# Kernel tuning notes

Measured on AMD Instinct MI355X. Metric: run time of the kernel, lower is better.

Reference implementation:

```python
import jax, jax.numpy as jnp
import numpy as np

D_MODEL = 1024
NUM_HEADS = 16
HEAD_DIM = D_MODEL // NUM_HEADS


def setup_inputs() -> dict:
    key = jax.random.key(0)
    ks = jax.random.split(key, 9)
    s = 1.0 / np.sqrt(D_MODEL)
    x = jax.random.normal(ks[0], (2, 2048, D_MODEL), dtype=jnp.float32)
    Wq = jax.random.uniform(ks[1], (D_MODEL, D_MODEL), jnp.float32, -s, s)
    bq = jax.random.uniform(ks[2], (D_MODEL,), jnp.float32, -s, s)
    Wk = jax.random.uniform(ks[3], (D_MODEL, D_MODEL), jnp.float32, -s, s)
    bk = jax.random.uniform(ks[4], (D_MODEL,), jnp.float32, -s, s)
    Wv = jax.random.uniform(ks[5], (D_MODEL, D_MODEL), jnp.float32, -s, s)
    bv = jax.random.uniform(ks[6], (D_MODEL,), jnp.float32, -s, s)
    Wo = jax.random.uniform(ks[7], (D_MODEL, D_MODEL), jnp.float32, -s, s)
    bo = jax.random.uniform(ks[8], (D_MODEL,), jnp.float32, -s, s)
    return {"x": x, "Wq": Wq, "bq": bq, "Wk": Wk, "bk": bk,
            "Wv": Wv, "bv": bv, "Wo": Wo, "bo": bo}


def reference(x, Wq, bq, Wk, bk, Wv, bv, Wo, bo):
    B, S, D = x.shape
    H, Hd = NUM_HEADS, HEAD_DIM
    # projections (torch Linear: x @ W.T + b; here W stored as [in, out])
    q = (x @ Wq + bq).reshape(B, S, H, Hd).transpose(0, 2, 1, 3)  # [B,H,S,Hd]
    k = (x @ Wk + bk).reshape(B, S, H, Hd).transpose(0, 2, 1, 3)
    v = (x @ Wv + bv).reshape(B, S, H, Hd).transpose(0, 2, 1, 3)
    scale = 1.0 / jnp.sqrt(jnp.asarray(Hd, dtype=x.dtype))
    scores = jnp.einsum('bhqd,bhkd->bhqk', q, k) * scale  # [B,H,S,S]
    attn = jax.nn.softmax(scores, axis=-1)
    out = jnp.einsum('bhqk,bhkd->bhqd', attn, v)  # [B,H,S,Hd]
    out = out.transpose(0, 2, 1, 3).reshape(B, S, D)
    return out @ Wo + bo
```

## Files before the change

kernel.cpp:

```cpp
#include <hip/hip_runtime.h>
#include <hip/hip_bf16.h>
#include <string.h>


#define DM 1024
#define S_LEN 2048
#define NH 16
#define HD 64

using u16 = unsigned short;
using u32 = unsigned int;

typedef short bf16x8 __attribute__((ext_vector_type(8)));
typedef float f32x4  __attribute__((ext_vector_type(4)));

__device__ __forceinline__ u16 f2bf(float f) {
    u32 i = __float_as_uint(f);
    u32 r = i + 0x7fffu + ((i >> 16) & 1u);
    return (u16)(r >> 16);
}
__device__ __forceinline__ u32 pk_bf16(float a, float b) {
    __hip_bfloat162 h = __float22bfloat162_rn(float2{a, b});
    u32 r; memcpy(&r, &h, 4);
    return r;
}

__global__ __launch_bounds__(256) void prep_x(const float* __restrict__ X, u16* __restrict__ out) {
    int i = (blockIdx.x * 256 + threadIdx.x) * 4;
    float4 v = *(const float4*)(X + i);
    *(uint2*)(out + i) = make_uint2(pk_bf16(v.x, v.y), pk_bf16(v.z, v.w));
}

__global__ __launch_bounds__(256) void prep_wt3(
    const float* __restrict__ W0, const float* __restrict__ W1, const float* __restrict__ W2,
    u16* __restrict__ T0, u16* __restrict__ T1, u16* __restrict__ T2)
{
    __shared__ u16 tile[64][72];
    const float* W = (blockIdx.z == 0) ? W0 : (blockIdx.z == 1) ? W1 : W2;
    u16* WT        = (blockIdx.z == 0) ? T0 : (blockIdx.z == 1) ? T1 : T2;
    const int t = threadIdx.x;
    const int n0 = blockIdx.x * 64, k0 = blockIdx.y * 64;
    #pragma unroll
    for (int it = 0; it < 4; it++) {
        int k = it * 16 + (t >> 4);
        int n = (t & 15) * 4;
        float4 v = *(const float4*)(W + (size_t)(k0 + k) * DM + n0 + n);
        tile[n + 0][k] = f2bf(v.x);
        tile[n + 1][k] = f2bf(v.y);
        tile[n + 2][k] = f2bf(v.z);
        tile[n + 3][k] = f2bf(v.w);
    }
    __syncthreads();
    int n = t >> 2, kg = (t & 3) * 16;
    uint4 a = *(const uint4*)&tile[n][kg];
    uint4 b = *(const uint4*)&tile[n][kg + 8];
    *(uint4*)(WT + (size_t)(n0 + n) * DM + k0 + kg)     = a;
    *(uint4*)(WT + (size_t)(n0 + n) * DM + k0 + kg + 8) = b;
}

__global__ __launch_bounds__(256) void prep_wt1(const float* __restrict__ W, u16* __restrict__ WT) {
    __shared__ u16 tile[64][72];
    const int t = threadIdx.x;
    const int n0 = blockIdx.x * 64, k0 = blockIdx.y * 64;
    #pragma unroll
    for (int it = 0; it < 4; it++) {
        int k = it * 16 + (t >> 4);
        int n = (t & 15) * 4;
        float4 v = *(const float4*)(W + (size_t)(k0 + k) * DM + n0 + n);
        tile[n + 0][k] = f2bf(v.x);
        tile[n + 1][k] = f2bf(v.y);
        tile[n + 2][k] = f2bf(v.z);
        tile[n + 3][k] = f2bf(v.w);
    }
    __syncthreads();
    int n = t >> 2, kg = (t & 3) * 16;
    uint4 a = *(const uint4*)&tile[n][kg];
    uint4 b = *(const uint4*)&tile[n][kg + 8];
    *(uint4*)(WT + (size_t)(n0 + n) * DM + k0 + kg)     = a;
    *(uint4*)(WT + (size_t)(n0 + n) * DM + k0 + kg + 8) = b;
}

__global__ __launch_bounds__(256) void gemm_qkv(
    const u16* __restrict__ WQT, const u16* __restrict__ WKT, const u16* __restrict__ WVT,
    const u16* __restrict__ X,
    const float* __restrict__ bq, const float* __restrict__ bk, const float* __restrict__ bv,
    u16* __restrict__ outQ, u16* __restrict__ outK, u16* __restrict__ outVT)
{
    __shared__ u16 Xs[128][72];
    __shared__ u16 Ws[3][64][72];

    const int t = threadIdx.x;
    const int w = t >> 6, lane = t & 63, quad = lane >> 4, l16 = lane & 15;
    const int Mb0 = blockIdx.x * 64;
    const int Nb0 = blockIdx.y * 128;
    const int Mb = Mb0 + (w & 1) * 32;
    const int Nb = Nb0 + (w >> 1) * 64;
    const int mloc = (w & 1) * 32, nloc = (w >> 1) * 64;

    f32x4 acc[3][2][4];
    #pragma unroll
    for (int q = 0; q < 3; q++)
        #pragma unroll
        for (int i = 0; i < 2; i++)
            #pragma unroll
            for (int j = 0; j < 4; j++) acc[q][i][j] = (f32x4){0.f, 0.f, 0.f, 0.f};

    const int sr = t >> 3, sc8 = (t & 7) * 8;

    for (int k0 = 0; k0 < DM; k0 += 64) {
        __syncthreads();
        #pragma unroll
        for (int i = 0; i < 4; i++) {
            int r = i * 32 + sr;
            *(uint4*)&Xs[r][sc8] =
                *(const uint4*)(X + (size_t)(Nb0 + r) * DM + k0 + sc8);
        }
        #pragma unroll
        for (int i = 0; i < 2; i++) {
            int r = i * 32 + sr;
            *(uint4*)&Ws[0][r][sc8] = *(const uint4*)(WQT + (size_t)(Mb0 + r) * DM + k0 + sc8);
            *(uint4*)&Ws[1][r][sc8] = *(const uint4*)(WKT + (size_t)(Mb0 + r) * DM + k0 + sc8);
            *(uint4*)&Ws[2][r][sc8] = *(const uint4*)(WVT + (size_t)(Mb0 + r) * DM + k0 + sc8);
        }
        __syncthreads();

        #pragma unroll
        for (int ks = 0; ks < 2; ks++) {
            const int kk = ks * 32 + quad * 8;
            bf16x8 bf[4];
            #pragma unroll
            for (int nt = 0; nt < 4; nt++)
                bf[nt] = *(const bf16x8*)&Xs[nloc + nt * 16 + l16][kk];
            bf16x8 aq0 = *(const bf16x8*)&Ws[0][mloc + l16][kk];
            bf16x8 aq1 = *(const bf16x8*)&Ws[0][mloc + 16 + l16][kk];
            bf16x8 ak0 = *(const bf16x8*)&Ws[1][mloc + l16][kk];
            bf16x8 ak1 = *(const bf16x8*)&Ws[1][mloc + 16 + l16][kk];
            bf16x8 av0 = *(const bf16x8*)&Ws[2][mloc + l16][kk];
            bf16x8 av1 = *(const bf16x8*)&Ws[2][mloc + 16 + l16][kk];
            #pragma unroll
            for (int nt = 0; nt < 4; nt++) {
                acc[0][0][nt] = __builtin_amdgcn_mfma_f32_16x16x32_bf16(aq0, bf[nt], acc[0][0][nt], 0, 0, 0);
                acc[0][1][nt] = __builtin_amdgcn_mfma_f32_16x16x32_bf16(aq1, bf[nt], acc[0][1][nt], 0, 0, 0);
                acc[1][0][nt] = __builtin_amdgcn_mfma_f32_16x16x32_bf16(ak0, bf[nt], acc[1][0][nt], 0, 0, 0);
                acc[1][1][nt] = __builtin_amdgcn_mfma_f32_16x16x32_bf16(ak1, bf[nt], acc[1][1][nt], 0, 0, 0);
                acc[2][0][nt] = __builtin_amdgcn_mfma_f32_16x16x32_bf16(av0, bf[nt], acc[2][0][nt], 0, 0, 0);
                acc[2][1][nt] = __builtin_amdgcn_mfma_f32_16x16x32_bf16(av1, bf[nt], acc[2][1][nt], 0, 0, 0);
            }
        }
    }

    const float QS = 0.18033688f;
    #pragma unroll
    for (int mt = 0; mt < 2; mt++) {
        int nf0 = Mb + mt * 16 + quad * 4;
        int h = nf0 >> 6, hd = nf0 & 63;
        float4 bvq = *(const float4*)(bq + nf0);
        float4 bvk = *(const float4*)(bk + nf0);
        #pragma unroll
        for (int nt = 0; nt < 4; nt++) {
            int m = Nb + nt * 16 + l16;
            int b = m >> 11, s = m & 2047;
            size_t idx = (size_t)(b * NH + h) * 131072 + (size_t)s * 64 + hd;
            *(uint2*)(outQ + idx) = make_uint2(
                pk_bf16((acc[0][mt][nt][0] + bvq.x) * QS, (acc[0][mt][nt][1] + bvq.y) * QS),
                pk_bf16((acc[0][mt][nt][2] + bvq.z) * QS, (acc[0][mt][nt][3] + bvq.w) * QS));
            *(uint2*)(outK + idx) = make_uint2(
                pk_bf16(acc[1][mt][nt][0] + bvk.x, acc[1][mt][nt][1] + bvk.y),
                pk_bf16(acc[1][mt][nt][2] + bvk.z, acc[1][mt][nt][3] + bvk.w));
        }
    }
    #pragma unroll
    for (int mt = 0; mt < 2; mt++) {
        #pragma unroll
        for (int r = 0; r < 4; r++) {
            int nf = Mb + mt * 16 + quad * 4 + r;
            int h = nf >> 6, hd = nf & 63;
            float bb = bv[nf];
            #pragma unroll
            for (int nt = 0; nt < 4; nt++) {
                int m = Nb + nt * 16 + l16;
                int b = m >> 11, s = m & 2047;
                outVT[(size_t)(b * NH + h) * 131072 + (size_t)hd * S_LEN + s]
                    = f2bf(acc[2][mt][nt][r] + bb);
            }
        }
    }
}

__global__ __launch_bounds__(256) void gemm_out(
    const u16* __restrict__ A, const u16* __restrict__ B,
    const float* __restrict__ bias, float* __restrict__ of32)
{
    __shared__ u16 As[64][72];
    __shared__ u16 Bs[128][72];

    const int t = threadIdx.x;
    const int w = t >> 6, lane = t & 63, quad = lane >> 4, l16 = lane & 15;
    const int Mb0 = blockIdx.x * 64;
    const int Nb0 = blockIdx.y * 128;
    const int Mb = Mb0 + (w & 1) * 32;
    const int Nb = Nb0 + (w >> 1) * 64;
    const int mloc = (w & 1) * 32, nloc = (w >> 1) * 64;

    f32x4 acc[2][4];
    #pragma unroll
    for (int i = 0; i < 2; i++)
        #pragma unroll
        for (int j = 0; j < 4; j++) acc[i][j] = (f32x4){0.f, 0.f, 0.f, 0.f};

    const int sr = t >> 3, sc8 = (t & 7) * 8;

    for (int k0 = 0; k0 < DM; k0 += 64) {
        const int h = k0 >> 6;
        __syncthreads();
        #pragma unroll
        for (int i = 0; i < 2; i++) {
            int r = i * 32 + sr;
            *(uint4*)&As[r][sc8] = *(const uint4*)(A + (size_t)(Mb0 + r) * DM + k0 + sc8);
        }
        #pragma unroll
        for (int i = 0; i < 4; i++) {
            int r = i * 32 + sr;
            int m = Nb0 + r;
            int b = m >> 11, s = m & 2047;
            *(uint4*)&Bs[r][sc8] =
                *(const uint4*)(B + (size_t)(b * NH + h) * 131072 + (size_t)s * 64 + sc8);
        }
        __syncthreads();

        #pragma unroll
        for (int ks = 0; ks < 2; ks++) {
            const int kk = ks * 32 + quad * 8;
            bf16x8 a0 = *(const bf16x8*)&As[mloc + l16][kk];
            bf16x8 a1 = *(const bf16x8*)&As[mloc + 16 + l16][kk];
            #pragma unroll
            for (int nt = 0; nt < 4; nt++) {
                bf16x8 bf = *(const bf16x8*)&Bs[nloc + nt * 16 + l16][kk];
                acc[0][nt] = __builtin_amdgcn_mfma_f32_16x16x32_bf16(a0, bf, acc[0][nt], 0, 0, 0);
                acc[1][nt] = __builtin_amdgcn_mfma_f32_16x16x32_bf16(a1, bf, acc[1][nt], 0, 0, 0);
            }
        }
    }
    #pragma unroll
    for (int mt = 0; mt < 2; mt++) {
        int nf0 = Mb + mt * 16 + quad * 4;
        float4 bvv = *(const float4*)(bias + nf0);
        #pragma unroll
        for (int nt = 0; nt < 4; nt++) {
            int m = Nb + nt * 16 + l16;
            float4 o;
            o.x = acc[mt][nt][0] + bvv.x; o.y = acc[mt][nt][1] + bvv.y;
            o.z = acc[mt][nt][2] + bvv.z; o.w = acc[mt][nt][3] + bvv.w;
            *(float4*)(of32 + (size_t)m * DM + nf0) = o;
        }
    }
}

__global__ __launch_bounds__(256) void attn_mfma(
    const u16* __restrict__ Q, const u16* __restrict__ K, const u16* __restrict__ VT,
    u16* __restrict__ O)
{
    __shared__ u16 Ks[64][72];
    __shared__ u16 Vs[64][72];
    __shared__ u16 P[64][72];

    const int t = threadIdx.x;
    const int w = t >> 6, lane = t & 63, quad = lane >> 4, l16 = lane & 15;
    const int bh = blockIdx.y;
    const int q0 = blockIdx.x * 64;
    const size_t base = (size_t)bh * 131072;

    bf16x8 qf[2];
    qf[0] = *(const bf16x8*)(Q + base + (size_t)(q0 + w * 16 + l16) * 64 + quad * 8);
    qf[1] = *(const bf16x8*)(Q + base + (size_t)(q0 + w * 16 + l16) * 64 + 32 + quad * 8);

    const short onebf = (short)0x3F80;
    const bf16x8 ones = {onebf, onebf, onebf, onebf, onebf, onebf, onebf, onebf};

    f32x4 o[4], lacc;
    #pragma unroll
    for (int i = 0; i < 4; i++) o[i] = (f32x4){0.f, 0.f, 0.f, 0.f};
    lacc = (f32x4){0.f, 0.f, 0.f, 0.f};

    for (int kt = 0; kt < 32; kt++) {
        __syncthreads();
        #pragma unroll
        for (int i = 0; i < 2; i++) {
            int f8 = i * 256 + t;
            int r = f8 >> 3, c8 = (f8 & 7) * 8;
            *(uint4*)&Ks[r][c8] = *(const uint4*)(K  + base + (size_t)(kt * 64 + r) * 64 + c8);
            *(uint4*)&Vs[r][c8] = *(const uint4*)(VT + base + (size_t)r * S_LEN + kt * 64 + c8);
        }
        __syncthreads();

        f32x4 sc[4];
        #pragma unroll
        for (int i = 0; i < 4; i++) sc[i] = (f32x4){0.f, 0.f, 0.f, 0.f};
        #pragma unroll
        for (int ks = 0; ks < 2; ks++)
            #pragma unroll
            for (int nt = 0; nt < 4; nt++) {
                bf16x8 kf = *(const bf16x8*)&Ks[nt * 16 + l16][ks * 32 + quad * 8];
                sc[nt] = __builtin_amdgcn_mfma_f32_16x16x32_bf16(qf[ks], kf, sc[nt], 0, 0, 0);
            }

        #pragma unroll
        for (int nt = 0; nt < 4; nt++) {
            float p0 = __builtin_amdgcn_exp2f(sc[nt][0]);
            float p1 = __builtin_amdgcn_exp2f(sc[nt][1]);
            float p2 = __builtin_amdgcn_exp2f(sc[nt][2]);
            float p3 = __builtin_amdgcn_exp2f(sc[nt][3]);
            u32 w01 = pk_bf16(p0, p1);
            u32 w23 = pk_bf16(p2, p3);
            const int row = w * 16 + quad * 4;
            const int col = nt * 16 + l16;
            P[row + 0][col] = (u16)(w01 & 0xffffu);
            P[row + 1][col] = (u16)(w01 >> 16);
            P[row + 2][col] = (u16)(w23 & 0xffffu);
            P[row + 3][col] = (u16)(w23 >> 16);
        }

        #pragma unroll
        for (int ks = 0; ks < 2; ks++) {
            bf16x8 pf = *(const bf16x8*)(&P[w * 16 + l16][ks * 32 + quad * 8]);
            lacc = __builtin_amdgcn_mfma_f32_16x16x32_bf16(pf, ones, lacc, 0, 0, 0);
            #pragma unroll
            for (int nt = 0; nt < 4; nt++) {
                bf16x8 vf = *(const bf16x8*)&Vs[nt * 16 + l16][ks * 32 + quad * 8];
                o[nt] = __builtin_amdgcn_mfma_f32_16x16x32_bf16(pf, vf, o[nt], 0, 0, 0);
            }
        }
    }

    #pragma unroll
    for (int r = 0; r < 4; r++) {
        float inv = 1.0f / lacc[r];
        int s = q0 + w * 16 + quad * 4 + r;
        #pragma unroll
        for (int nt = 0; nt < 4; nt++)
            O[base + (size_t)s * 64 + nt * 16 + l16] = f2bf(o[nt][r] * inv);
    }
}

extern "C" void kernel_launch(void* const* d_in, const int* in_sizes, int n_in,
                              void* d_out, int out_size, void* d_ws, size_t ws_size,
                              hipStream_t stream) {
    const float* x  = (const float*)d_in[0];
    const float* Wq = (const float*)d_in[1];
    const float* bq = (const float*)d_in[2];
    const float* Wk = (const float*)d_in[3];
    const float* bk = (const float*)d_in[4];
    const float* Wv = (const float*)d_in[5];
    const float* bv = (const float*)d_in[6];
    const float* Wo = (const float*)d_in[7];
    const float* bo = (const float*)d_in[8];
    float* out = (float*)d_out;

    u16* xbf = (u16*)d_out;
    u16* wqt = xbf + 4194304;
    u16* wkt = wqt + 1048576;
    u16* wvt = wkt + 1048576;

    u16* qws  = (u16*)d_ws;
    u16* kws  = qws + 4194304;
    u16* vtws = kws + 4194304;
    u16* wot  = kws;

    prep_x<<<4096, 256, 0, stream>>>(x, xbf);
    prep_wt3<<<dim3(16, 16, 3), 256, 0, stream>>>(Wq, Wk, Wv, wqt, wkt, wvt);

    gemm_qkv<<<dim3(16, 32), 256, 0, stream>>>(wqt, wkt, wvt, xbf, bq, bk, bv,
                                               qws, kws, vtws);

    attn_mfma<<<dim3(32, 32), 256, 0, stream>>>(qws, kws, vtws, qws);

    prep_wt1<<<dim3(16, 16), 256, 0, stream>>>(Wo, wot);
    gemm_out<<<dim3(16, 32), 256, 0, stream>>>(wot, qws, bo, out);
}
```

Measured before the change: 227.9 us.

## Double-buffer K/V tiles in attention and widen blocks to 128 queries

The attention kernel now uses 512 threads covering 128 query rows per block. Each K/V tile is staged once in LDS and shared by twice as many waves. The next K/V tile is prefetched into registers while the current tile's MFMAs run, then written into the alternate LDS buffer. That cuts the loop to one barrier per iteration and hides global load latency. In exchange, LDS use per block roughly doubles and the grid halves, which may lower occupancy or the number of resident blocks.

```diff
diff --git a/kernel.cpp b/kernel.cpp
--- a/kernel.cpp
+++ b/kernel.cpp
@@ -256,18 +256,18 @@
     }
 }
 
-__global__ __launch_bounds__(256) void attn_mfma(
+__global__ __launch_bounds__(512) void attn_mfma(
     const u16* __restrict__ Q, const u16* __restrict__ K, const u16* __restrict__ VT,
     u16* __restrict__ O)
 {
-    __shared__ u16 Ks[64][72];
-    __shared__ u16 Vs[64][72];
-    __shared__ u16 P[64][72];
+    __shared__ u16 Ks[2][64][72];
+    __shared__ u16 Vs[2][64][72];
+    __shared__ u16 P[128][72];
 
     const int t = threadIdx.x;
     const int w = t >> 6, lane = t & 63, quad = lane >> 4, l16 = lane & 15;
     const int bh = blockIdx.y;
-    const int q0 = blockIdx.x * 64;
+    const int q0 = blockIdx.x * 128;
     const size_t base = (size_t)bh * 131072;
 
     bf16x8 qf[2];
@@ -282,16 +282,26 @@
     for (int i = 0; i < 4; i++) o[i] = (f32x4){0.f, 0.f, 0.f, 0.f};
     lacc = (f32x4){0.f, 0.f, 0.f, 0.f};
 
+    const int sr = t >> 3;
+    const int sc8 = (t & 7) * 8;
+    const u16* Kg = K + base;
+    const u16* Vg = VT + base;
+
+    {
+        uint4 k0v = *(const uint4*)(Kg + (size_t)sr * 64 + sc8);
+        uint4 v0v = *(const uint4*)(Vg + (size_t)sr * S_LEN + sc8);
+        *(uint4*)&Ks[0][sr][sc8] = k0v;
+        *(uint4*)&Vs[0][sr][sc8] = v0v;
+    }
+    __syncthreads();
+
+    uint4 kreg, vreg;
     for (int kt = 0; kt < 32; kt++) {
-        __syncthreads();
-        #pragma unroll
-        for (int i = 0; i < 2; i++) {
-            int f8 = i * 256 + t;
-            int r = f8 >> 3, c8 = (f8 & 7) * 8;
-            *(uint4*)&Ks[r][c8] = *(const uint4*)(K  + base + (size_t)(kt * 64 + r) * 64 + c8);
-            *(uint4*)&Vs[r][c8] = *(const uint4*)(VT + base + (size_t)r * S_LEN + kt * 64 + c8);
-        }
-        __syncthreads();
+        const int cur = kt & 1;
+        if (kt < 31) {
+            kreg = *(const uint4*)(Kg + (size_t)((kt + 1) * 64 + sr) * 64 + sc8);
+            vreg = *(const uint4*)(Vg + (size_t)sr * S_LEN + (kt + 1) * 64 + sc8);
+        }
 
         f32x4 sc[4];
         #pragma unroll
@@ -300,7 +310,7 @@
         for (int ks = 0; ks < 2; ks++)
             #pragma unroll
             for (int nt = 0; nt < 4; nt++) {
-                bf16x8 kf = *(const bf16x8*)&Ks[nt * 16 + l16][ks * 32 + quad * 8];
+                bf16x8 kf = *(const bf16x8*)&Ks[cur][nt * 16 + l16][ks * 32 + quad * 8];
                 sc[nt] = __builtin_amdgcn_mfma_f32_16x16x32_bf16(qf[ks], kf, sc[nt], 0, 0, 0);
             }
 
@@ -326,10 +336,16 @@
             lacc = __builtin_amdgcn_mfma_f32_16x16x32_bf16(pf, ones, lacc, 0, 0, 0);
             #pragma unroll
             for (int nt = 0; nt < 4; nt++) {
-                bf16x8 vf = *(const bf16x8*)&Vs[nt * 16 + l16][ks * 32 + quad * 8];
+                bf16x8 vf = *(const bf16x8*)&Vs[cur][nt * 16 + l16][ks * 32 + quad * 8];
                 o[nt] = __builtin_amdgcn_mfma_f32_16x16x32_bf16(pf, vf, o[nt], 0, 0, 0);
             }
         }
+
+        if (kt < 31) {
+            *(uint4*)&Ks[cur ^ 1][sr][sc8] = kreg;
+            *(uint4*)&Vs[cur ^ 1][sr][sc8] = vreg;
+        }
+        __syncthreads();
     }
 
     #pragma unroll
@@ -372,7 +388,7 @@
     gemm_qkv<<<dim3(16, 32), 256, 0, stream>>>(wqt, wkt, wvt, xbf, bq, bk, bv,
                                                qws, kws, vtws);
 
-    attn_mfma<<<dim3(32, 32), 256, 0, stream>>>(qws, kws, vtws, qws);
+    attn_mfma<<<dim3(16, 32), 512, 0, stream>>>(qws, kws, vtws, qws);
 
     prep_wt1<<<dim3(16, 16), 256, 0, stream>>>(Wo, wot);
     gemm_out<<<dim3(16, 32), 256, 0, stream>>>(wot, qws, bo, out);
```

Result: faster. 214.0 us (-6.1%).
